# Performance work log

Hardware: AMD Instinct MI355X
Metric: run time of the kernel (lower is better)

The kernel has to match this reference:

```python
import math
import jax, jax.numpy as jnp
import numpy as np

B, C, H, W = 8, 512, 32, 32
N_HEADS = 8
N_GROUPS = 32  # GroupNorm(32) as in guided-diffusion normalization()
EPS = 1e-5


def setup_inputs() -> dict:
    key = jax.random.key(0)
    k0, k1, k2, k3, k4 = jax.random.split(key, 5)
    x = jax.random.normal(k0, (B, C, H, W), dtype=jnp.float32)
    gn_scale = jnp.ones((C,), dtype=jnp.float32)
    gn_bias = jnp.zeros((C,), dtype=jnp.float32)
    # 1x1 conv weights stored as (out, in); proj_out is zero-initialized in the
    # original but we use small random weights so the op is non-trivial.
    qkv_w = jax.random.normal(k1, (3 * C, C), dtype=jnp.float32) * 0.02
    qkv_b = jax.random.normal(k2, (3 * C,), dtype=jnp.float32) * 0.02
    proj_w = jax.random.normal(k3, (C, C), dtype=jnp.float32) * 0.02
    proj_b = jax.random.normal(k4, (C,), dtype=jnp.float32) * 0.02
    return {"x": x, "gn_scale": gn_scale, "gn_bias": gn_bias,
            "qkv_w": qkv_w, "qkv_b": qkv_b, "proj_w": proj_w, "proj_b": proj_b}


def reference(x, gn_scale, gn_bias, qkv_w, qkv_b, proj_w, proj_b):
    b, c, h, w = x.shape
    L = h * w
    xf = x.reshape(b, c, L)

    # GroupNorm(32): normalize over (channels-in-group, length)
    xg = xf.reshape(b, N_GROUPS, c // N_GROUPS, L)
    mu = jnp.mean(xg, axis=(2, 3), keepdims=True)
    var = jnp.var(xg, axis=(2, 3), keepdims=True)
    xn = ((xg - mu) * jax.lax.rsqrt(var + EPS)).reshape(b, c, L)
    xn = xn * gn_scale[None, :, None] + gn_bias[None, :, None]

    # 1x1 conv -> qkv (b, 3c, L)
    qkv = jnp.einsum('oc,bcl->bol', qkv_w, xn) + qkv_b[None, :, None]

    ch = c // N_HEADS  # head dim (width//(3*n_heads) of qkv)
    q, k, v = jnp.split(qkv, 3, axis=1)
    q = q.reshape(b * N_HEADS, ch, L)
    k = k.reshape(b * N_HEADS, ch, L)
    v = v.reshape(b * N_HEADS, ch, L)

    scale = 1.0 / math.sqrt(math.sqrt(ch))
    # scores: (b*heads, L, L) materialized, as in the original
    wts = jnp.einsum('bct,bcs->bts', q * scale, k * scale)
    wts = jax.nn.softmax(wts.astype(jnp.float32), axis=-1).astype(q.dtype)
    a = jnp.einsum('bts,bcs->bct', wts, v).reshape(b, c, L)

    # zero-initialized 1x1 proj in original; random weights here
    hout = jnp.einsum('oc,bcl->bol', proj_w, a) + proj_b[None, :, None]
    return (xf + hout).reshape(b, c, h, w)
```

## Files before the change

### kernel.cpp

```cpp
#include <hip/hip_runtime.h>
#include <math.h>

#define BATCH   8
#define CCH     512
#define LL      1024
#define NHEADS  8
#define CHD     64
#define EPSV    1e-5f
#define QSCALE  0.1803368801111204f

typedef __bf16 bf16_t;
typedef bf16_t bf16x8 __attribute__((ext_vector_type(8)));
typedef bf16_t bf16x4 __attribute__((ext_vector_type(4)));
typedef float  f32x4  __attribute__((ext_vector_type(4)));

__device__ __forceinline__ bf16_t f2b(float f) {
  unsigned u = __float_as_uint(f);
  u += 0x7fff + ((u >> 16) & 1);
  return __builtin_bit_cast(bf16_t, (unsigned short)(u >> 16));
}

__device__ __forceinline__ unsigned pack2(float lo, float hi) {
  unsigned a = (unsigned)__builtin_bit_cast(unsigned short, f2b(lo));
  unsigned b = (unsigned)__builtin_bit_cast(unsigned short, f2b(hi));
  return (b << 16) | a;
}

__device__ __forceinline__ void gload_lds16(const void* g, void* l) {
  __builtin_amdgcn_global_load_lds(
      (const __attribute__((address_space(1))) void*)g,
      (__attribute__((address_space(3))) void*)l, 16, 0, 0);
}

__global__ __launch_bounds__(256) void gn_norm(const float* __restrict__ x,
                                               const float* __restrict__ gsc,
                                               const float* __restrict__ gbi,
                                               bf16_t* __restrict__ xnT) {
  int lin = blockIdx.x;
  int xcd = lin & 7, slot = lin >> 3;
  int b = slot & 7, jj = slot >> 3;
  int g = xcd * 4 + jj;
  const float4* x4 = (const float4*)(x + ((size_t)(b * 32 + g)) * 16 * LL);
  int tid = threadIdx.x;

  float s = 0.f, ss = 0.f;
  float4 v[16];
#pragma unroll
  for (int it = 0; it < 16; ++it) {
    float4 f = x4[it * 256 + tid];
    v[it] = f;
    s += f.x + f.y + f.z + f.w;
    ss += f.x * f.x + f.y * f.y + f.z * f.z + f.w * f.w;
  }
#pragma unroll
  for (int m = 1; m < 64; m <<= 1) { s += __shfl_xor(s, m); ss += __shfl_xor(ss, m); }
  __shared__ float rs_[4], rss[4];
  int wv = tid >> 6, ln = tid & 63;
  if (ln == 0) { rs_[wv] = s; rss[wv] = ss; }
  __syncthreads();
  s  = rs_[0] + rs_[1] + rs_[2] + rs_[3];
  ss = rss[0] + rss[1] + rss[2] + rss[3];
  float mean = s * (1.f / 16384.f);
  float var  = ss * (1.f / 16384.f) - mean * mean;
  float rstd = rsqrtf(var + EPSV);

  float sc[16], bi[16];
#pragma unroll
  for (int it = 0; it < 16; ++it) {
    sc[it] = gsc[g * 16 + it] * rstd;
    bi[it] = gbi[g * 16 + it] - mean * sc[it];
  }

#pragma unroll
  for (int j = 0; j < 4; ++j) {
    unsigned w[8];
#pragma unroll
    for (int k = 0; k < 8; ++k) {
      float a0 = (j == 0 ? v[2 * k].x : j == 1 ? v[2 * k].y : j == 2 ? v[2 * k].z : v[2 * k].w);
      float a1 = (j == 0 ? v[2 * k + 1].x : j == 1 ? v[2 * k + 1].y : j == 2 ? v[2 * k + 1].z : v[2 * k + 1].w);
      w[k] = pack2(a0 * sc[2 * k] + bi[2 * k], a1 * sc[2 * k + 1] + bi[2 * k + 1]);
    }
    int l = tid * 4 + j;
    bf16_t* dst = xnT + ((size_t)b * LL + l) * CCH + g * 16;
    *(uint4*)dst = make_uint4(w[0], w[1], w[2], w[3]);
    *(uint4*)(dst + 8) = make_uint4(w[4], w[5], w[6], w[7]);
  }
}

__global__ __launch_bounds__(256) void cvt_bf16(const float* __restrict__ src,
                                                bf16_t* __restrict__ dst, int n) {
  int i = (blockIdx.x * 256 + threadIdx.x) * 4;
  if (i < n) {
    float4 v = *(const float4*)(src + i);
    bf16x4 o = {f2b(v.x), f2b(v.y), f2b(v.z), f2b(v.w)};
    *(bf16x4*)(dst + i) = o;
  }
}

__global__ __launch_bounds__(256) void qkv_mfma(const bf16_t* __restrict__ wq,
                                                const bf16_t* __restrict__ xnT,
                                                const float* __restrict__ qkvb,
                                                bf16_t* __restrict__ qt,
                                                bf16_t* __restrict__ kt,
                                                bf16_t* __restrict__ vt) {
  __shared__ bf16_t As[128 * 64];
  __shared__ bf16_t Bs[128 * 64];
  int tid = threadIdx.x;
  int wave = tid >> 6, lane = tid & 63;
  int lrow = lane & 15, quad = lane >> 4;
  int wm = wave >> 1, wn = wave & 1;
  int b = blockIdx.x;
  int oBase = blockIdx.y * 128, lBase = blockIdx.z * 128;
  int srow = lane >> 3;
  int sgOff = (((lane & 7) ^ srow) << 4);

  f32x4 acc[4][4] = {};
  for (int ktile = 0; ktile < 8; ++ktile) {
    int kB = ktile * 64;
    __syncthreads();
#pragma unroll
    for (int j = 0; j < 4; ++j) {
      int ci = wave * 4 + j;
      int R = ci * 8 + srow;
      gload_lds16((const char*)(wq + (size_t)(oBase + R) * CCH + kB) + sgOff,
                  (char*)As + ci * 1024);
      gload_lds16((const char*)(xnT + ((size_t)b * LL + lBase + R) * CCH + kB) + sgOff,
                  (char*)Bs + ci * 1024);
    }
    __syncthreads();
#pragma unroll
    for (int kk = 0; kk < 2; ++kk) {
      bf16x8 af[4], bfr[4];
#pragma unroll
      for (int m = 0; m < 4; ++m) {
        int r = wm * 64 + m * 16 + lrow;
        int g = (kk * 4 + quad) ^ (lrow & 7);
        af[m] = *(const bf16x8*)(As + r * 64 + g * 8);
      }
#pragma unroll
      for (int n = 0; n < 4; ++n) {
        int r = wn * 64 + n * 16 + lrow;
        int g = (kk * 4 + quad) ^ (lrow & 7);
        bfr[n] = *(const bf16x8*)(Bs + r * 64 + g * 8);
      }
#pragma unroll
      for (int m = 0; m < 4; ++m)
#pragma unroll
        for (int n = 0; n < 4; ++n)
          acc[m][n] = __builtin_amdgcn_mfma_f32_16x16x32_bf16(af[m], bfr[n], acc[m][n], 0, 0, 0);
    }
  }

  int oW = oBase + wm * 64;
  int lW = lBase + wn * 64;
  int sec = oW >> 9;
#pragma unroll
  for (int m = 0; m < 4; ++m) {
    int o4 = oW + m * 16 + quad * 4;
    float4 bb4 = *(const float4*)&qkvb[o4];
    int cc = o4 & 511;
    int head = cc >> 6, ch = cc & 63;
    int bh = b * NHEADS + head;
    if (sec == 0) {
#pragma unroll
      for (int n = 0; n < 4; ++n) {
        int l = lW + n * 16 + lrow;
        unsigned d0 = pack2((acc[m][n][0] + bb4.x) * QSCALE,
                            (acc[m][n][1] + bb4.y) * QSCALE);
        unsigned d1 = pack2((acc[m][n][2] + bb4.z) * QSCALE,
                            (acc[m][n][3] + bb4.w) * QSCALE);
        *(uint2*)(qt + ((size_t)bh * LL + l) * CHD + ch) = make_uint2(d0, d1);
      }
    } else if (sec == 1) {
#pragma unroll
      for (int n = 0; n < 4; ++n) {
        int l = lW + n * 16 + lrow;
        unsigned d0 = pack2(acc[m][n][0] + bb4.x, acc[m][n][1] + bb4.y);
        unsigned d1 = pack2(acc[m][n][2] + bb4.z, acc[m][n][3] + bb4.w);
        *(uint2*)(kt + ((size_t)bh * LL + l) * CHD + ch) = make_uint2(d0, d1);
      }
    } else {
      float bb[4] = {bb4.x, bb4.y, bb4.z, bb4.w};
#pragma unroll
      for (int i = 0; i < 4; ++i) {
        unsigned d0 = pack2(acc[m][0][i] + bb[i], acc[m][1][i] + bb[i]);
        unsigned d1 = pack2(acc[m][2][i] + bb[i], acc[m][3][i] + bb[i]);
        *(uint2*)(vt + ((size_t)bh * CHD + ch + i) * LL + lW + lrow * 4) =
            make_uint2(d0, d1);
      }
    }
  }
}

__global__ __launch_bounds__(256) void attn_mfma(const bf16_t* __restrict__ qt,
                                                 const bf16_t* __restrict__ kt,
                                                 const bf16_t* __restrict__ vt,
                                                 bf16_t* __restrict__ at) {
  __shared__ bf16_t kbuf[2][64 * 64];
  __shared__ bf16_t vbuf[2][64 * 64];
  __shared__ bf16_t pb[8 * 16 * 72];
  int tid = threadIdx.x, wave = tid >> 6, lane = tid & 63;
  int lrow = lane & 15, quad = lane >> 4;
  int bh = blockIdx.x;
  int tW = blockIdx.y * 128 + wave * 32;
  const bf16_t* qb = qt + (size_t)bh * LL * CHD;
  const bf16_t* kb = kt + (size_t)bh * LL * CHD;
  const bf16_t* vb = vt + (size_t)bh * CHD * LL;

  int srow = lane >> 3;
  int sgb = (((lane & 7) ^ srow) << 4);

  bf16x8 qf[2][2];
#pragma unroll
  for (int h = 0; h < 2; ++h) {
    const bf16_t* qp = qb + (size_t)(tW + h * 16 + lrow) * CHD + quad * 8;
    qf[h][0] = *(const bf16x8*)qp;
    qf[h][1] = *(const bf16x8*)(qp + 32);
  }

  bf16x8 ones;
#pragma unroll
  for (int j = 0; j < 8; ++j) ones[j] = (bf16_t)1.0f;

  f32x4 Oa[2][4] = {};
  f32x4 Os[2] = {};

#pragma unroll
  for (int j = 0; j < 2; ++j) {
    int c = wave * 2 + j;
    int R = c * 8 + srow;
    gload_lds16((const char*)(kb + (size_t)R * CHD) + sgb, (char*)&kbuf[0][0] + c * 1024);
    gload_lds16((const char*)(vb + (size_t)R * LL) + sgb, (char*)&vbuf[0][0] + c * 1024);
  }
  __syncthreads();

  int swz0 = (quad ^ (lrow & 7)) * 8;
  int swz1 = ((quad + 4) ^ (lrow & 7)) * 8;

  for (int st = 0; st < 16; ++st) {
    int cur = st & 1;
    if (st < 15) {
      int sBn = (st + 1) * 64;
#pragma unroll
      for (int j = 0; j < 2; ++j) {
        int c = wave * 2 + j;
        int R = c * 8 + srow;
        gload_lds16((const char*)(kb + (size_t)(sBn + R) * CHD) + sgb,
                    (char*)&kbuf[cur ^ 1][0] + c * 1024);
        gload_lds16((const char*)(vb + (size_t)R * LL + sBn) + sgb,
                    (char*)&vbuf[cur ^ 1][0] + c * 1024);
      }
    }
    const bf16_t* kbase = &kbuf[cur][0];
    const bf16_t* vbase = &vbuf[cur][0];

    f32x4 S[2][4];
#pragma unroll
    for (int ss = 0; ss < 4; ++ss) {
      int s = ss * 16 + lrow;
      bf16x8 k0 = *(const bf16x8*)(kbase + s * 64 + swz0);
      bf16x8 k1 = *(const bf16x8*)(kbase + s * 64 + swz1);
#pragma unroll
      for (int h = 0; h < 2; ++h) {
        f32x4 z = {0.f, 0.f, 0.f, 0.f};
        z = __builtin_amdgcn_mfma_f32_16x16x32_bf16(qf[h][0], k0, z, 0, 0, 0);
        S[h][ss] = __builtin_amdgcn_mfma_f32_16x16x32_bf16(qf[h][1], k1, z, 0, 0, 0);
      }
    }

#pragma unroll
    for (int h = 0; h < 2; ++h) {
      bf16_t* pw = pb + (wave * 2 + h) * (16 * 72);
      float p[4][4];
#pragma unroll
      for (int ss = 0; ss < 4; ++ss)
#pragma unroll
        for (int i = 0; i < 4; ++i)
          p[ss][i] = __builtin_amdgcn_exp2f(S[h][ss][i]);
#pragma unroll
      for (int i = 0; i < 4; ++i) {
        unsigned d0 = __builtin_amdgcn_perm(__float_as_uint(p[1][i]),
                                            __float_as_uint(p[0][i]), 0x07060302u);
        unsigned d1 = __builtin_amdgcn_perm(__float_as_uint(p[3][i]),
                                            __float_as_uint(p[2][i]), 0x07060302u);
        uint2* dst = (uint2*)(pw + (quad * 4 + i) * 72 + lrow * 4);
        *dst = make_uint2(d0, d1);
      }
    }
    asm volatile("s_waitcnt lgkmcnt(0)" ::: "memory");

    bf16x8 pf[2][2];
#pragma unroll
    for (int h = 0; h < 2; ++h) {
      const bf16_t* pw = pb + (wave * 2 + h) * (16 * 72);
      pf[h][0] = *(const bf16x8*)(pw + lrow * 72 + quad * 8);
      pf[h][1] = *(const bf16x8*)(pw + lrow * 72 + 32 + quad * 8);
    }

#pragma unroll
    for (int n = 0; n < 4; ++n) {
      int r = (n * 16 + lrow) * 64;
      bf16x8 v0 = *(const bf16x8*)(vbase + r + swz0);
      bf16x8 v1 = *(const bf16x8*)(vbase + r + swz1);
#pragma unroll
      for (int h = 0; h < 2; ++h) {
        Oa[h][n] = __builtin_amdgcn_mfma_f32_16x16x32_bf16(pf[h][0], v0, Oa[h][n], 0, 0, 0);
        Oa[h][n] = __builtin_amdgcn_mfma_f32_16x16x32_bf16(pf[h][1], v1, Oa[h][n], 0, 0, 0);
      }
    }
#pragma unroll
    for (int h = 0; h < 2; ++h) {
      Os[h] = __builtin_amdgcn_mfma_f32_16x16x32_bf16(pf[h][0], ones, Os[h], 0, 0, 0);
      Os[h] = __builtin_amdgcn_mfma_f32_16x16x32_bf16(pf[h][1], ones, Os[h], 0, 0, 0);
    }

    __syncthreads();
  }

  bf16_t* ab = at + (size_t)bh * LL * CHD;
#pragma unroll
  for (int h = 0; h < 2; ++h) {
    float inv[4];
#pragma unroll
    for (int i = 0; i < 4; ++i) inv[i] = 1.f / Os[h][i];
#pragma unroll
    for (int n = 0; n < 4; ++n)
#pragma unroll
      for (int i = 0; i < 4; ++i)
        ab[(size_t)(tW + h * 16 + quad * 4 + i) * CHD + n * 16 + lrow] =
            f2b(Oa[h][n][i] * inv[i]);
  }
}

__global__ __launch_bounds__(256) void proj_mfma(const bf16_t* __restrict__ wp,
                                                 const bf16_t* __restrict__ at,
                                                 const float* __restrict__ projb,
                                                 const float* __restrict__ x,
                                                 float* __restrict__ out) {
  __shared__ bf16_t As[128 * 64];
  __shared__ bf16_t Bs[128 * 64];
  int tid = threadIdx.x;
  int wave = tid >> 6, lane = tid & 63;
  int lrow = lane & 15, quad = lane >> 4;
  int wm = wave >> 1, wn = wave & 1;
  int b = blockIdx.x;
  int oBase = blockIdx.y * 128, lBase = blockIdx.z * 128;
  int srow = lane >> 3;
  int sgOff = (((lane & 7) ^ srow) << 4);

  f32x4 acc[4][4] = {};
  for (int ktile = 0; ktile < 8; ++ktile) {
    int kB = ktile * 64;
    __syncthreads();
#pragma unroll
    for (int j = 0; j < 4; ++j) {
      int ci = wave * 4 + j;
      int R = ci * 8 + srow;
      gload_lds16((const char*)(wp + (size_t)(oBase + R) * CCH + kB) + sgOff,
                  (char*)As + ci * 1024);
      gload_lds16((const char*)(at + ((size_t)(b * NHEADS + ktile) * LL + lBase + R) * CHD) + sgOff,
                  (char*)Bs + ci * 1024);
    }
    __syncthreads();
#pragma unroll
    for (int kk = 0; kk < 2; ++kk) {
      bf16x8 af[4], bfr[4];
#pragma unroll
      for (int m = 0; m < 4; ++m) {
        int r = wm * 64 + m * 16 + lrow;
        int g = (kk * 4 + quad) ^ (lrow & 7);
        af[m] = *(const bf16x8*)(As + r * 64 + g * 8);
      }
#pragma unroll
      for (int n = 0; n < 4; ++n) {
        int r = wn * 64 + n * 16 + lrow;
        int g = (kk * 4 + quad) ^ (lrow & 7);
        bfr[n] = *(const bf16x8*)(Bs + r * 64 + g * 8);
      }
#pragma unroll
      for (int m = 0; m < 4; ++m)
#pragma unroll
        for (int n = 0; n < 4; ++n)
          acc[m][n] = __builtin_amdgcn_mfma_f32_16x16x32_bf16(af[m], bfr[n], acc[m][n], 0, 0, 0);
    }
  }

  int oW = oBase + wm * 64;
  int lW = lBase + wn * 64;
#pragma unroll
  for (int m = 0; m < 4; ++m) {
#pragma unroll
    for (int i = 0; i < 4; ++i) {
      int o = oW + m * 16 + quad * 4 + i;
      float bb = projb[o];
#pragma unroll
      for (int n = 0; n < 4; ++n) {
        int l = lW + n * 16 + lrow;
        size_t off = ((size_t)(b * CCH + o)) * LL + l;
        out[off] = acc[m][n][i] + bb + x[off];
      }
    }
  }
}

extern "C" void kernel_launch(void* const* d_in, const int* in_sizes, int n_in,
                              void* d_out, int out_size, void* d_ws, size_t ws_size,
                              hipStream_t stream) {
  const float* x     = (const float*)d_in[0];
  const float* gsc   = (const float*)d_in[1];
  const float* gbi   = (const float*)d_in[2];
  const float* qkvw  = (const float*)d_in[3];
  const float* qkvb  = (const float*)d_in[4];
  const float* projw = (const float*)d_in[5];
  const float* projb = (const float*)d_in[6];
  float* out = (float*)d_out;

  char* ws = (char*)d_ws;
  bf16_t* wqb   = (bf16_t*)(ws + 4096);
  bf16_t* wpb   = (bf16_t*)(ws + 4096 + 1572864);
  bf16_t* xnT   = (bf16_t*)(ws + 2101248);
  bf16_t* qt    = (bf16_t*)(ws + 2101248 + 8388608);
  bf16_t* kt    = (bf16_t*)(ws + 2101248 + 2 * 8388608);
  bf16_t* vt    = (bf16_t*)(ws + 2101248 + 3 * 8388608);
  bf16_t* at    = (bf16_t*)(ws + 2101248 + 4 * 8388608);

  hipLaunchKernelGGL(cvt_bf16, dim3(768), dim3(256), 0, stream, qkvw, wqb, 1536 * 512);
  hipLaunchKernelGGL(cvt_bf16, dim3(256), dim3(256), 0, stream, projw, wpb, 512 * 512);
  hipLaunchKernelGGL(gn_norm, dim3(256), dim3(256), 0, stream, x, gsc, gbi, xnT);
  hipLaunchKernelGGL(qkv_mfma, dim3(BATCH, 12, 8), dim3(256), 0, stream,
                     wqb, xnT, qkvb, qt, kt, vt);
  hipLaunchKernelGGL(attn_mfma, dim3(64, 8), dim3(256), 0, stream, qt, kt, vt, at);
  hipLaunchKernelGGL(proj_mfma, dim3(BATCH, 4, 8), dim3(256), 0, stream,
                     wpb, at, projb, x, out);
}
```

Baseline: 162.3 us.

## Load K/V attention fragments directly from global memory into registers; merge weight conversions

```diff
diff --git a/kernel.cpp b/kernel.cpp
--- a/kernel.cpp
+++ b/kernel.cpp
@@ -87,14 +87,19 @@
   }
 }
 
-__global__ __launch_bounds__(256) void cvt_bf16(const float* __restrict__ src,
-                                                bf16_t* __restrict__ dst, int n) {
+__global__ __launch_bounds__(256) void cvt_both(const float* __restrict__ qkvw,
+                                                const float* __restrict__ projw,
+                                                bf16_t* __restrict__ wqb,
+                                                bf16_t* __restrict__ wpb) {
   int i = (blockIdx.x * 256 + threadIdx.x) * 4;
-  if (i < n) {
-    float4 v = *(const float4*)(src + i);
-    bf16x4 o = {f2b(v.x), f2b(v.y), f2b(v.z), f2b(v.w)};
-    *(bf16x4*)(dst + i) = o;
-  }
+  const float* src;
+  bf16_t* dst;
+  int j;
+  if (i < 1536 * 512) { src = qkvw; dst = wqb; j = i; }
+  else                { src = projw; dst = wpb; j = i - 1536 * 512; }
+  float4 v = *(const float4*)(src + j);
+  bf16x4 o = {f2b(v.x), f2b(v.y), f2b(v.z), f2b(v.w)};
+  *(bf16x4*)(dst + j) = o;
 }
 
 __global__ __launch_bounds__(256) void qkv_mfma(const bf16_t* __restrict__ wq,
@@ -192,12 +197,10 @@
   }
 }
 
-__global__ __launch_bounds__(256) void attn_mfma(const bf16_t* __restrict__ qt,
-                                                 const bf16_t* __restrict__ kt,
-                                                 const bf16_t* __restrict__ vt,
-                                                 bf16_t* __restrict__ at) {
-  __shared__ bf16_t kbuf[2][64 * 64];
-  __shared__ bf16_t vbuf[2][64 * 64];
+__global__ __launch_bounds__(256, 2) void attn_mfma(const bf16_t* __restrict__ qt,
+                                                    const bf16_t* __restrict__ kt,
+                                                    const bf16_t* __restrict__ vt,
+                                                    bf16_t* __restrict__ at) {
   __shared__ bf16_t pb[8 * 16 * 72];
   int tid = threadIdx.x, wave = tid >> 6, lane = tid & 63;
   int lrow = lane & 15, quad = lane >> 4;
@@ -207,9 +210,6 @@
   const bf16_t* kb = kt + (size_t)bh * LL * CHD;
   const bf16_t* vb = vt + (size_t)bh * CHD * LL;
 
-  int srow = lane >> 3;
-  int sgb = (((lane & 7) ^ srow) << 4);
-
   bf16x8 qf[2][2];
 #pragma unroll
   for (int h = 0; h < 2; ++h) {
@@ -225,47 +225,42 @@
   f32x4 Oa[2][4] = {};
   f32x4 Os[2] = {};
 
-#pragma unroll
-  for (int j = 0; j < 2; ++j) {
-    int c = wave * 2 + j;
-    int R = c * 8 + srow;
-    gload_lds16((const char*)(kb + (size_t)R * CHD) + sgb, (char*)&kbuf[0][0] + c * 1024);
-    gload_lds16((const char*)(vb + (size_t)R * LL) + sgb, (char*)&vbuf[0][0] + c * 1024);
-  }
-  __syncthreads();
-
-  int swz0 = (quad ^ (lrow & 7)) * 8;
-  int swz1 = ((quad + 4) ^ (lrow & 7)) * 8;
+  bf16x8 kf0[4], kf1[4];
+#pragma unroll
+  for (int ss = 0; ss < 4; ++ss) {
+    const bf16_t* kp = kb + (size_t)(ss * 16 + lrow) * CHD + quad * 8;
+    kf0[ss] = *(const bf16x8*)kp;
+    kf1[ss] = *(const bf16x8*)(kp + 32);
+  }
 
   for (int st = 0; st < 16; ++st) {
-    int cur = st & 1;
-    if (st < 15) {
-      int sBn = (st + 1) * 64;
-#pragma unroll
-      for (int j = 0; j < 2; ++j) {
-        int c = wave * 2 + j;
-        int R = c * 8 + srow;
-        gload_lds16((const char*)(kb + (size_t)(sBn + R) * CHD) + sgb,
-                    (char*)&kbuf[cur ^ 1][0] + c * 1024);
-        gload_lds16((const char*)(vb + (size_t)R * LL + sBn) + sgb,
-                    (char*)&vbuf[cur ^ 1][0] + c * 1024);
-      }
-    }
-    const bf16_t* kbase = &kbuf[cur][0];
-    const bf16_t* vbase = &vbuf[cur][0];
+    int sB = st * 64;
+
+    bf16x8 vf0[4], vf1[4];
+#pragma unroll
+    for (int n = 0; n < 4; ++n) {
+      const bf16_t* vp = vb + (size_t)(n * 16 + lrow) * LL + sB + quad * 8;
+      vf0[n] = *(const bf16x8*)vp;
+      vf1[n] = *(const bf16x8*)(vp + 32);
+    }
 
     f32x4 S[2][4];
 #pragma unroll
     for (int ss = 0; ss < 4; ++ss) {
-      int s = ss * 16 + lrow;
-      bf16x8 k0 = *(const bf16x8*)(kbase + s * 64 + swz0);
-      bf16x8 k1 = *(const bf16x8*)(kbase + s * 64 + swz1);
 #pragma unroll
       for (int h = 0; h < 2; ++h) {
         f32x4 z = {0.f, 0.f, 0.f, 0.f};
-        z = __builtin_amdgcn_mfma_f32_16x16x32_bf16(qf[h][0], k0, z, 0, 0, 0);
-        S[h][ss] = __builtin_amdgcn_mfma_f32_16x16x32_bf16(qf[h][1], k1, z, 0, 0, 0);
-      }
+        z = __builtin_amdgcn_mfma_f32_16x16x32_bf16(qf[h][0], kf0[ss], z, 0, 0, 0);
+        S[h][ss] = __builtin_amdgcn_mfma_f32_16x16x32_bf16(qf[h][1], kf1[ss], z, 0, 0, 0);
+      }
+    }
+
+    int sBn = (st < 15) ? sB + 64 : 0;
+#pragma unroll
+    for (int ss = 0; ss < 4; ++ss) {
+      const bf16_t* kp = kb + (size_t)(sBn + ss * 16 + lrow) * CHD + quad * 8;
+      kf0[ss] = *(const bf16x8*)kp;
+      kf1[ss] = *(const bf16x8*)(kp + 32);
     }
 
 #pragma unroll
@@ -299,13 +294,10 @@
 
 #pragma unroll
     for (int n = 0; n < 4; ++n) {
-      int r = (n * 16 + lrow) * 64;
-      bf16x8 v0 = *(const bf16x8*)(vbase + r + swz0);
-      bf16x8 v1 = *(const bf16x8*)(vbase + r + swz1);
 #pragma unroll
       for (int h = 0; h < 2; ++h) {
-        Oa[h][n] = __builtin_amdgcn_mfma_f32_16x16x32_bf16(pf[h][0], v0, Oa[h][n], 0, 0, 0);
-        Oa[h][n] = __builtin_amdgcn_mfma_f32_16x16x32_bf16(pf[h][1], v1, Oa[h][n], 0, 0, 0);
+        Oa[h][n] = __builtin_amdgcn_mfma_f32_16x16x32_bf16(pf[h][0], vf0[n], Oa[h][n], 0, 0, 0);
+        Oa[h][n] = __builtin_amdgcn_mfma_f32_16x16x32_bf16(pf[h][1], vf1[n], Oa[h][n], 0, 0, 0);
       }
     }
 #pragma unroll
@@ -313,8 +305,6 @@
       Os[h] = __builtin_amdgcn_mfma_f32_16x16x32_bf16(pf[h][0], ones, Os[h], 0, 0, 0);
       Os[h] = __builtin_amdgcn_mfma_f32_16x16x32_bf16(pf[h][1], ones, Os[h], 0, 0, 0);
     }
-
-    __syncthreads();
   }
 
   bf16_t* ab = at + (size_t)bh * LL * CHD;
@@ -424,8 +414,7 @@
   bf16_t* vt    = (bf16_t*)(ws + 2101248 + 3 * 8388608);
   bf16_t* at    = (bf16_t*)(ws + 2101248 + 4 * 8388608);
 
-  hipLaunchKernelGGL(cvt_bf16, dim3(768), dim3(256), 0, stream, qkvw, wqb, 1536 * 512);
-  hipLaunchKernelGGL(cvt_bf16, dim3(256), dim3(256), 0, stream, projw, wpb, 512 * 512);
+  hipLaunchKernelGGL(cvt_both, dim3(1024), dim3(256), 0, stream, qkvw, projw, wqb, wpb);
   hipLaunchKernelGGL(gn_norm, dim3(256), dim3(256), 0, stream, x, gsc, gbi, xnT);
   hipLaunchKernelGGL(qkv_mfma, dim3(BATCH, 12, 8), dim3(256), 0, stream,
                      wqb, xnT, qkvb, qt, kt, vt);
```

Result: slower. 190.7 us (+17.5%).

## Fuse weight conversion with groupnorm and load V fragments directly from global

Applied to the files above, without the earlier changes.

```diff
diff --git a/kernel.cpp b/kernel.cpp
--- a/kernel.cpp
+++ b/kernel.cpp
@@ -32,16 +32,33 @@
       (__attribute__((address_space(3))) void*)l, 16, 0, 0);
 }
 
-__global__ __launch_bounds__(256) void gn_norm(const float* __restrict__ x,
-                                               const float* __restrict__ gsc,
-                                               const float* __restrict__ gbi,
-                                               bf16_t* __restrict__ xnT) {
-  int lin = blockIdx.x;
+__global__ __launch_bounds__(256) void prep_fused(const float* __restrict__ qkvw,
+                                                  const float* __restrict__ projw,
+                                                  bf16_t* __restrict__ wqb,
+                                                  bf16_t* __restrict__ wpb,
+                                                  const float* __restrict__ x,
+                                                  const float* __restrict__ gsc,
+                                                  const float* __restrict__ gbi,
+                                                  bf16_t* __restrict__ xnT) {
+  int bid = blockIdx.x;
+  int tid = threadIdx.x;
+  if (bid < 1024) {
+    int i = (bid * 256 + tid) * 4;
+    const float* src;
+    bf16_t* dst;
+    int j;
+    if (i < 1536 * 512) { src = qkvw; dst = wqb; j = i; }
+    else                { src = projw; dst = wpb; j = i - 1536 * 512; }
+    float4 v = *(const float4*)(src + j);
+    bf16x4 o = {f2b(v.x), f2b(v.y), f2b(v.z), f2b(v.w)};
+    *(bf16x4*)(dst + j) = o;
+    return;
+  }
+  int lin = bid - 1024;
   int xcd = lin & 7, slot = lin >> 3;
   int b = slot & 7, jj = slot >> 3;
   int g = xcd * 4 + jj;
   const float4* x4 = (const float4*)(x + ((size_t)(b * 32 + g)) * 16 * LL);
-  int tid = threadIdx.x;
 
   float s = 0.f, ss = 0.f;
   float4 v[16];
@@ -84,16 +101,6 @@
     bf16_t* dst = xnT + ((size_t)b * LL + l) * CCH + g * 16;
     *(uint4*)dst = make_uint4(w[0], w[1], w[2], w[3]);
     *(uint4*)(dst + 8) = make_uint4(w[4], w[5], w[6], w[7]);
-  }
-}
-
-__global__ __launch_bounds__(256) void cvt_bf16(const float* __restrict__ src,
-                                                bf16_t* __restrict__ dst, int n) {
-  int i = (blockIdx.x * 256 + threadIdx.x) * 4;
-  if (i < n) {
-    float4 v = *(const float4*)(src + i);
-    bf16x4 o = {f2b(v.x), f2b(v.y), f2b(v.z), f2b(v.w)};
-    *(bf16x4*)(dst + i) = o;
   }
 }
 
@@ -197,7 +204,6 @@
                                                  const bf16_t* __restrict__ vt,
                                                  bf16_t* __restrict__ at) {
   __shared__ bf16_t kbuf[2][64 * 64];
-  __shared__ bf16_t vbuf[2][64 * 64];
   __shared__ bf16_t pb[8 * 16 * 72];
   int tid = threadIdx.x, wave = tid >> 6, lane = tid & 63;
   int lrow = lane & 15, quad = lane >> 4;
@@ -230,7 +236,6 @@
     int c = wave * 2 + j;
     int R = c * 8 + srow;
     gload_lds16((const char*)(kb + (size_t)R * CHD) + sgb, (char*)&kbuf[0][0] + c * 1024);
-    gload_lds16((const char*)(vb + (size_t)R * LL) + sgb, (char*)&vbuf[0][0] + c * 1024);
   }
   __syncthreads();
 
@@ -239,20 +244,27 @@
 
   for (int st = 0; st < 16; ++st) {
     int cur = st & 1;
+    int sB = st * 64;
+
+    bf16x8 vf0[4], vf1[4];
+#pragma unroll
+    for (int n = 0; n < 4; ++n) {
+      const bf16_t* vp = vb + (size_t)(n * 16 + lrow) * LL + sB + quad * 8;
+      vf0[n] = *(const bf16x8*)vp;
+      vf1[n] = *(const bf16x8*)(vp + 32);
+    }
+
     if (st < 15) {
-      int sBn = (st + 1) * 64;
+      int sBn = sB + 64;
 #pragma unroll
       for (int j = 0; j < 2; ++j) {
         int c = wave * 2 + j;
         int R = c * 8 + srow;
         gload_lds16((const char*)(kb + (size_t)(sBn + R) * CHD) + sgb,
                     (char*)&kbuf[cur ^ 1][0] + c * 1024);
-        gload_lds16((const char*)(vb + (size_t)R * LL + sBn) + sgb,
-                    (char*)&vbuf[cur ^ 1][0] + c * 1024);
       }
     }
     const bf16_t* kbase = &kbuf[cur][0];
-    const bf16_t* vbase = &vbuf[cur][0];
 
     f32x4 S[2][4];
 #pragma unroll
@@ -299,13 +311,10 @@
 
 #pragma unroll
     for (int n = 0; n < 4; ++n) {
-      int r = (n * 16 + lrow) * 64;
-      bf16x8 v0 = *(const bf16x8*)(vbase + r + swz0);
-      bf16x8 v1 = *(const bf16x8*)(vbase + r + swz1);
 #pragma unroll
       for (int h = 0; h < 2; ++h) {
-        Oa[h][n] = __builtin_amdgcn_mfma_f32_16x16x32_bf16(pf[h][0], v0, Oa[h][n], 0, 0, 0);
-        Oa[h][n] = __builtin_amdgcn_mfma_f32_16x16x32_bf16(pf[h][1], v1, Oa[h][n], 0, 0, 0);
+        Oa[h][n] = __builtin_amdgcn_mfma_f32_16x16x32_bf16(pf[h][0], vf0[n], Oa[h][n], 0, 0, 0);
+        Oa[h][n] = __builtin_amdgcn_mfma_f32_16x16x32_bf16(pf[h][1], vf1[n], Oa[h][n], 0, 0, 0);
       }
     }
 #pragma unroll
@@ -424,9 +433,8 @@
   bf16_t* vt    = (bf16_t*)(ws + 2101248 + 3 * 8388608);
   bf16_t* at    = (bf16_t*)(ws + 2101248 + 4 * 8388608);
 
-  hipLaunchKernelGGL(cvt_bf16, dim3(768), dim3(256), 0, stream, qkvw, wqb, 1536 * 512);
-  hipLaunchKernelGGL(cvt_bf16, dim3(256), dim3(256), 0, stream, projw, wpb, 512 * 512);
-  hipLaunchKernelGGL(gn_norm, dim3(256), dim3(256), 0, stream, x, gsc, gbi, xnT);
+  hipLaunchKernelGGL(prep_fused, dim3(1280), dim3(256), 0, stream,
+                     qkvw, projw, wqb, wpb, x, gsc, gbi, xnT);
   hipLaunchKernelGGL(qkv_mfma, dim3(BATCH, 12, 8), dim3(256), 0, stream,
                      wqb, xnT, qkvb, qt, kt, vt);
   hipLaunchKernelGGL(attn_mfma, dim3(64, 8), dim3(256), 0, stream, qt, kt, vt, at);
```

Measured after the change: 166.0 us. +2.3%, slower.
